# Kernel optimization log

Hardware: AMD Instinct MI355X
Metric: run time of the kernel (lower is better)

Reference implementation:

```python
import jax, jax.numpy as jnp
import numpy as np

B, L, H = 4, 1024, 8192
NH, HD = 64, 128
PD = HD // 2  # 64, rope-style positional dim
QL = HD * 4 * 3  # 1536, Q latent dim
KVL = HD * 4     # 512, KV latent dim


def setup_inputs() -> dict:
    key = jax.random.key(0)
    ks = jax.random.split(key, 18)
    w = lambda k, i, o: (jax.random.normal(k, (i, o), jnp.float32) * (1.0 / np.sqrt(i))).astype(jnp.float32)
    b = lambda k, o: jnp.zeros((o,), jnp.float32)
    return {
        'x': jax.random.normal(ks[0], (B, L, H), jnp.float32),
        'W_dq': w(ks[1], H, QL),   'b_dq': b(ks[2], QL),
        'W_dkv': w(ks[3], H, KVL), 'b_dkv': b(ks[4], KVL),
        'W_uq': w(ks[5], QL, H),   'b_uq': b(ks[6], H),
        'W_uk': w(ks[7], KVL, H),  'b_uk': b(ks[8], H),
        'W_uv': w(ks[9], KVL, H),  'b_uv': b(ks[10], H),
        'W_pq': w(ks[11], QL, NH * PD), 'b_pq': b(ks[12], NH * PD),
        'W_pk': w(ks[13], H, PD),  'b_pk': b(ks[14], PD),
        'W_o': w(ks[15], H, H),    'b_o': b(ks[16], H),
    }


def reference(x, W_dq, b_dq, W_dkv, b_dkv, W_uq, b_uq, W_uk, b_uk,
              W_uv, b_uv, W_pq, b_pq, W_pk, b_pk, W_o, b_o):
    Bb, Ll, Hh = x.shape
    # low-rank latents
    Q_lat = x @ W_dq + b_dq          # (B, L, 1536)
    KV_lat = x @ W_dkv + b_dkv       # (B, L, 512)
    # up-projections
    Q_c = (Q_lat @ W_uq + b_uq).reshape(Bb, Ll, NH, HD)
    Q_r = (Q_lat @ W_pq + b_pq).reshape(Bb, Ll, NH, PD)
    Q = jnp.concatenate([Q_c, Q_r], axis=-1)            # (B, L, NH, 192)
    K_c = (KV_lat @ W_uk + b_uk).reshape(Bb, Ll, NH, HD)
    K_r = x @ W_pk + b_pk                                # (B, L, 64), shared across heads
    K_r = jnp.broadcast_to(K_r[:, :, None, :], (Bb, Ll, NH, PD))
    K = jnp.concatenate([K_c, K_r], axis=-1)             # (B, L, NH, 192)
    V = (KV_lat @ W_uv + b_uv).reshape(Bb, Ll, NH, HD)   # (B, L, NH, 128)
    # attention with mismatched Q/K (192) vs V (128) head dims; scale by sqrt(128)
    scores = jnp.einsum('bqhd,bkhd->bhqk', Q, K) / np.float32(np.sqrt(HD))
    causal = jnp.tril(jnp.ones((Ll, Ll), bool))
    scores = jnp.where(causal, scores, jnp.float32(-jnp.inf))
    attn = jax.nn.softmax(scores, axis=-1)               # dropout = identity (eval)
    out = jnp.einsum('bhqk,bkhd->bqhd', attn, V).reshape(Bb, Ll, Hh)
    return out @ W_o + b_o
```

## Files before the change

### kernel.cpp

```cpp
#include <hip/hip_runtime.h>
#include <cstdint>

typedef unsigned short u16;
typedef __attribute__((ext_vector_type(8))) short bf16x8;
typedef __attribute__((ext_vector_type(4))) float f32x4;
typedef __attribute__((ext_vector_type(4))) unsigned short u16x4;

__device__ __forceinline__ u16 f2b(float f) {
  union { float f; uint32_t u; } v; v.f = f;
  uint32_t r = v.u + 0x7FFFu + ((v.u >> 16) & 1u);
  return (u16)(r >> 16);
}

__device__ __forceinline__ void gload_lds16(const void* g, void* l) {
  __builtin_amdgcn_global_load_lds((const __attribute__((address_space(1))) void*)g,
                                   (__attribute__((address_space(3))) void*)l, 16, 0, 0);
}

__device__ __forceinline__ void barrier_raw() {
  __builtin_amdgcn_sched_barrier(0);
  asm volatile("" ::: "memory");
  __builtin_amdgcn_s_barrier();
  asm volatile("" ::: "memory");
  __builtin_amdgcn_sched_barrier(0);
}
__device__ __forceinline__ void wait_vm8() {
  asm volatile("s_waitcnt vmcnt(8)" ::: "memory");
  __builtin_amdgcn_sched_barrier(0);
}

__global__ __launch_bounds__(256) void cvt_bf16(const float* __restrict__ in,
                                                u16* __restrict__ out, long n) {
  long i = ((long)blockIdx.x * 256 + threadIdx.x) * 4;
  if (i >= n) return;
  f32x4 v = *(const f32x4*)(in + i);
  u16x4 o;
#pragma unroll
  for (int k = 0; k < 4; k++) o[k] = f2b(v[k]);
  *(u16x4*)(out + i) = o;
}

__global__ __launch_bounds__(256) void transpose_cvt(const float* __restrict__ W,
                                                     u16* __restrict__ WT, int K, int N) {
  __shared__ float tile[32][33];
  const int tn0 = blockIdx.x * 32;
  const int tk0 = blockIdx.y * 32;
  const int c = threadIdx.x & 31;
  const int r0 = threadIdx.x >> 5;
#pragma unroll
  for (int rr = 0; rr < 32; rr += 8)
    tile[r0 + rr][c] = W[(long)(tk0 + r0 + rr) * N + tn0 + c];
  __syncthreads();
#pragma unroll
  for (int rr = 0; rr < 32; rr += 8)
    WT[(long)(tn0 + r0 + rr) * K + tk0 + c] = f2b(tile[c][r0 + rr]);
}

__global__ __launch_bounds__(256) void biascat(const float* __restrict__ a,
                                               const float* __restrict__ b,
                                               const float* __restrict__ c,
                                               float* __restrict__ o) {
  int i = blockIdx.x * 256 + threadIdx.x;
  if (i < 1536) o[i] = a[i];
  else if (i < 2048) o[i] = b[i - 1536];
  else if (i < 2112) o[i] = c[i - 2048];
}

__global__ __launch_bounds__(256) void repl_kr(const u16* __restrict__ Kr,
                                               u16* __restrict__ Kbuf, int stride) {
  long idx = (long)blockIdx.x * 256 + threadIdx.x;
  int d4 = idx & 15;
  long t = idx >> 4;
  int hh = t & 63;
  long tok = t >> 6;
  if (tok >= 4096) return;
  u16x4 v = *(const u16x4*)(Kr + tok * (long)stride + d4 * 4);
  long b = tok >> 10, l = tok & 1023;
  *(u16x4*)(Kbuf + ((b * 64 + hh) * 1024 + l) * 192 + 128 + d4 * 4) = v;
}

template<int MODE>
__global__ __launch_bounds__(512, 2) void gemm256(
    const u16* __restrict__ A, long lda, const u16* __restrict__ BT,
    const float* __restrict__ bias, void* __restrict__ outp,
    int N, int K, int p0, int p1) {
  __shared__ u16 sA[2][2][8192];
  __shared__ u16 sB[2][2][8192];
  const int tid = threadIdx.x;
  const int lane = tid & 63;
  const int w = tid >> 6;
  const int wr = w >> 2, wc = w & 3;
  const int hi = lane >> 4, lo = lane & 15;

  const int Nt = gridDim.x, Mt = gridDim.y;
  const int bid = blockIdx.y * Nt + blockIdx.x;
  const int xcd = bid & 7;
  const int idx = bid >> 3;
  int mt, nt;
  if ((Nt & 1) == 0) {
    const int Rm = Mt >> 2, Rn = Nt >> 1;
    const int xr = xcd & 3, xcn = xcd >> 2;
    const int Wb = Rn < 8 ? Rn : 8;
    const int cb = idx / (Rm * Wb);
    const int rem = idx - cb * (Rm * Wb);
    mt = xr * Rm + (rem % Rm);
    nt = xcn * Rn + cb * Wb + rem / Rm;
  } else {
    const int Rm = Mt >> 3;
    const int Wb = Nt < 8 ? Nt : 8;
    const int cb = idx / (Rm * Wb);
    const int rem = idx - cb * (Rm * Wb);
    mt = xcd * Rm + (rem % Rm);
    nt = cb * Wb + rem / Rm;
  }
  const long m0 = (long)mt * 256;
  const long n0 = (long)nt * 256;

  const int nkt = K >> 6;

  const int srow = tid >> 2;
  const int scol = ((tid & 3) ^ ((tid >> 3) & 3)) * 8;
  const long arow0 = m0 + srow, arow1 = arow0 + 128;
  long brow0 = n0 + srow, brow1 = brow0 + 128;
  if (brow0 > N - 1) brow0 = N - 1;
  if (brow1 > N - 1) brow1 = N - 1;
  const u16* aS0 = A + arow0 * lda + scol;
  const u16* aS1 = A + arow1 * lda + scol;
  const u16* bS0 = BT + brow0 * (long)K + scol;
  const u16* bS1 = BT + brow1 * (long)K + scol;

  const int aRd = (wr * 128 + lo) * 32 + (hi ^ ((lo >> 1) & 3)) * 8;
  const int bRd = (wc * 64 + lo) * 32 + (hi ^ ((lo >> 1) & 3)) * 8;

  f32x4 acc[8][4] = {};

#define STAGE(s0, s1, koff, dst) do { \
    gload_lds16((s0) + (koff), (dst) + tid * 8); \
    gload_lds16((s1) + (koff), (dst) + 4096 + tid * 8); \
  } while (0)
#define LDA_F(bufr, kh, m) (*(const bf16x8*)(&sA[bufr][kh][aRd + (m) * 512]))
#define LDB_F(bufr, kh, n) (*(const bf16x8*)(&sB[bufr][kh][bRd + (n) * 512]))
#define MFMA_GRP(mi, av) \
    acc[mi][0] = __builtin_amdgcn_mfma_f32_16x16x32_bf16(av, b0, acc[mi][0], 0, 0, 0); \
    acc[mi][1] = __builtin_amdgcn_mfma_f32_16x16x32_bf16(av, b1, acc[mi][1], 0, 0, 0); \
    acc[mi][2] = __builtin_amdgcn_mfma_f32_16x16x32_bf16(av, b2, acc[mi][2], 0, 0, 0); \
    acc[mi][3] = __builtin_amdgcn_mfma_f32_16x16x32_bf16(av, b3, acc[mi][3], 0, 0, 0);

  STAGE(aS0, aS1, 0, &sA[0][0][0]);
  STAGE(bS0, bS1, 0, &sB[0][0][0]);
  STAGE(aS0, aS1, 32, &sA[0][1][0]);
  STAGE(bS0, bS1, 32, &sB[0][1][0]);
  {
    const long t1o = (nkt > 1) ? 64 : 0;
    STAGE(aS0, aS1, t1o, &sA[1][0][0]);
    STAGE(bS0, bS1, t1o, &sB[1][0][0]);
  }
  asm volatile("s_waitcnt vmcnt(4)" ::: "memory");
  __builtin_amdgcn_sched_barrier(0);
  barrier_raw();

  for (int t = 0; t < nkt; ++t) {
    const int cur = t & 1, nxt = cur ^ 1;
    const int t1c = (t + 1 < nkt) ? t + 1 : nkt - 1;
    const int t2c = (t + 2 < nkt) ? t + 2 : nkt - 1;
    const long o1 = (long)t1c * 64;
    const long o2 = (long)t2c * 64;
    bf16x8 b0, b1, b2, b3, a0, a1, a2, a3;
    b0 = LDB_F(cur, 0, 0); b1 = LDB_F(cur, 0, 1); b2 = LDB_F(cur, 0, 2); b3 = LDB_F(cur, 0, 3);
    a0 = LDA_F(cur, 0, 0); a1 = LDA_F(cur, 0, 1); a2 = LDA_F(cur, 0, 2); a3 = LDA_F(cur, 0, 3);
    STAGE(aS0, aS1, o1 + 32, &sA[nxt][1][0]);
    barrier_raw();
    __builtin_amdgcn_s_setprio(1);
    MFMA_GRP(0, a0) MFMA_GRP(1, a1) MFMA_GRP(2, a2) MFMA_GRP(3, a3)
    __builtin_amdgcn_s_setprio(0);
    barrier_raw();
    a0 = LDA_F(cur, 0, 4); a1 = LDA_F(cur, 0, 5); a2 = LDA_F(cur, 0, 6); a3 = LDA_F(cur, 0, 7);
    STAGE(bS0, bS1, o1 + 32, &sB[nxt][1][0]);
    barrier_raw();
    __builtin_amdgcn_s_setprio(1);
    MFMA_GRP(4, a0) MFMA_GRP(5, a1) MFMA_GRP(6, a2) MFMA_GRP(7, a3)
    __builtin_amdgcn_s_setprio(0);
    wait_vm8();
    barrier_raw();
    b0 = LDB_F(cur, 1, 0); b1 = LDB_F(cur, 1, 1); b2 = LDB_F(cur, 1, 2); b3 = LDB_F(cur, 1, 3);
    a0 = LDA_F(cur, 1, 0); a1 = LDA_F(cur, 1, 1); a2 = LDA_F(cur, 1, 2); a3 = LDA_F(cur, 1, 3);
    STAGE(aS0, aS1, o2, &sA[cur][0][0]);
    barrier_raw();
    __builtin_amdgcn_s_setprio(1);
    MFMA_GRP(0, a0) MFMA_GRP(1, a1) MFMA_GRP(2, a2) MFMA_GRP(3, a3)
    __builtin_amdgcn_s_setprio(0);
    barrier_raw();
    a0 = LDA_F(cur, 1, 4); a1 = LDA_F(cur, 1, 5); a2 = LDA_F(cur, 1, 6); a3 = LDA_F(cur, 1, 7);
    STAGE(bS0, bS1, o2, &sB[cur][0][0]);
    barrier_raw();
    __builtin_amdgcn_s_setprio(1);
    MFMA_GRP(4, a0) MFMA_GRP(5, a1) MFMA_GRP(6, a2) MFMA_GRP(7, a3)
    __builtin_amdgcn_s_setprio(0);
    wait_vm8();
    barrier_raw();
  }
  asm volatile("s_waitcnt vmcnt(0)" ::: "memory");

#undef STAGE
#undef LDA_F
#undef LDB_F
#undef MFMA_GRP

#pragma unroll
  for (int m = 0; m < 8; m++) {
#pragma unroll
    for (int n = 0; n < 4; n++) {
      const long mb = m0 + wr * 128 + m * 16 + hi * 4;
      const long nn = n0 + wc * 64 + n * 16 + lo;
      if (nn >= N) continue;
      const float bv = bias[nn];
      if (MODE == 2) {
        u16x4 pk;
#pragma unroll
        for (int r = 0; r < 4; r++) pk[r] = f2b(acc[m][n][r] + bv);
        const long bq = mb >> 10, l = mb & 1023;
        const long h = nn >> 7, d = nn & 127;
        *(u16x4*)((u16*)outp + ((bq * 64 + h) * 128 + d) * 1024 + l) = pk;
      } else if (MODE == 1) {
#pragma unroll
        for (int r = 0; r < 4; r++) {
          const long mm = mb + r;
          const long bq = mm >> 10, l = mm & 1023;
          const long h = nn >> p0, d = nn & ((1 << p0) - 1);
          ((u16*)outp)[((bq * 64 + h) * 1024 + l) * 192 + p1 + d] = f2b(acc[m][n][r] + bv);
        }
      } else if (MODE == 3) {
#pragma unroll
        for (int r = 0; r < 4; r++)
          ((float*)outp)[(mb + r) * (long)N + nn] = acc[m][n][r] + bv;
      } else {
#pragma unroll
        for (int r = 0; r < 4; r++)
          ((u16*)outp)[(mb + r) * (long)N + nn] = f2b(acc[m][n][r] + bv);
      }
    }
  }
}

__global__ __launch_bounds__(512, 2) void attn256(const u16* __restrict__ Qb,
                                                  const u16* __restrict__ Kb,
                                                  const u16* __restrict__ Vt,
                                                  u16* __restrict__ O) {
  __shared__ u16 sK[2][12288];
  __shared__ u16 sV[2][8192];
  __shared__ u16 P[8][32][72];
  const int bh = blockIdx.x;
  const int qtb = 3 - blockIdx.y;
  const int b = bh >> 6, h = bh & 63;
  const int tid = threadIdx.x, w = tid >> 6, lane = tid & 63;
  const int hi = lane >> 4, lo = lane & 15, lo7 = lane & 7;
  const int q0w = qtb * 256 + w * 32;
  const u16* Qh = Qb + (size_t)bh * 1024 * 192;
  const u16* Kh = Kb + (size_t)bh * 1024 * 192;
  const u16* Vh = Vt + (size_t)bh * 128 * 1024;
  const float scale = 0.08838834764831845f;
  const float NEGINF = -3.0e38f;

  int kOff0, kOff1, kOff2, vOff0, vOff1;
  {
    int g0 = tid, g1 = tid + 512, g2 = tid + 1024;
    int r0 = g0 / 24, r1 = g1 / 24, r2 = g2 / 24;
    kOff0 = r0 * 192 + ((g0 - r0 * 24) ^ (r0 & 7)) * 8;
    kOff1 = r1 * 192 + ((g1 - r1 * 24) ^ (r1 & 7)) * 8;
    kOff2 = r2 * 192 + ((g2 - r2 * 24) ^ (r2 & 7)) * 8;
    int s0 = tid, s1 = tid + 512;
    vOff0 = (s0 >> 3) * 1024 + ((s0 & 7) ^ ((s0 >> 3) & 7)) * 8;
    vOff1 = (s1 >> 3) * 1024 + ((s1 & 7) ^ ((s1 >> 3) & 7)) * 8;
  }
#define STAGE_KV(tt, bb) do { \
    const u16* kb_ = Kh + (size_t)(tt) * (64 * 192); \
    const u16* vb_ = Vh + (size_t)(tt) * 64; \
    gload_lds16(kb_ + kOff0, &sK[bb][0] + tid * 8); \
    gload_lds16(kb_ + kOff1, &sK[bb][4096] + tid * 8); \
    gload_lds16(kb_ + kOff2, &sK[bb][8192] + tid * 8); \
    gload_lds16(vb_ + vOff0, &sV[bb][0] + tid * 8); \
    gload_lds16(vb_ + vOff1, &sV[bb][4096] + tid * 8); \
  } while (0)

  bf16x8 qf[2][6];
#pragma unroll
  for (int qi = 0; qi < 2; qi++) {
    const u16* qp = Qh + (size_t)(q0w + qi * 16 + lo) * 192 + hi * 8;
#pragma unroll
    for (int f = 0; f < 6; f++) qf[qi][f] = *(const bf16x8*)(qp + f * 32);
  }

  f32x4 oacc[2][8] = {};
  float m_run[2][4], l_run[2][4];
#pragma unroll
  for (int qi = 0; qi < 2; qi++)
#pragma unroll
    for (int r = 0; r < 4; r++) { m_run[qi][r] = NEGINF; l_run[qi][r] = 0.f; }

  const int nkt = (qtb + 1) * 4;
  STAGE_KV(0, 0);
  __syncthreads();

  for (int t = 0; t < nkt; t++) {
    const int cur = t & 1;
    const int tn = (t + 1 < nkt) ? t + 1 : nkt - 1;
    STAGE_KV(tn, cur ^ 1);
    const int k0 = t * 64;
    if (k0 < q0w + 32) {
      f32x4 s[2][4] = {};
      __builtin_amdgcn_s_setprio(1);
#pragma unroll
      for (int j = 0; j < 4; j++) {
#pragma unroll
        for (int f = 0; f < 6; f++) {
          bf16x8 kf = *(const bf16x8*)(&sK[cur][((j * 16 + lo) * 24 + ((f * 4 + hi) ^ lo7)) * 8]);
          s[0][j] = __builtin_amdgcn_mfma_f32_16x16x32_bf16(qf[0][f], kf, s[0][j], 0, 0, 0);
          s[1][j] = __builtin_amdgcn_mfma_f32_16x16x32_bf16(qf[1][f], kf, s[1][j], 0, 0, 0);
        }
      }
      __builtin_amdgcn_s_setprio(0);
      const bool diag = (k0 + 63 > q0w);
#pragma unroll
      for (int qi = 0; qi < 2; qi++) {
#pragma unroll
        for (int r = 0; r < 4; r++) {
          const int q = q0w + qi * 16 + hi * 4 + r;
          float sv[4];
          float mx = NEGINF;
#pragma unroll
          for (int j = 0; j < 4; j++) {
            float v = s[qi][j][r] * scale;
            if (diag && (k0 + j * 16 + lo > q)) v = NEGINF;
            sv[j] = v;
            mx = fmaxf(mx, v);
          }
#pragma unroll
          for (int o = 1; o < 16; o <<= 1) mx = fmaxf(mx, __shfl_xor(mx, o, 64));
          const float mnew = fmaxf(m_run[qi][r], mx);
          float sum = 0.f;
#pragma unroll
          for (int j = 0; j < 4; j++) {
            float pv = __expf(sv[j] - mnew);
            sum += pv;
            P[w][qi * 16 + hi * 4 + r][j * 16 + lo] = f2b(pv);
          }
#pragma unroll
          for (int o = 1; o < 16; o <<= 1) sum += __shfl_xor(sum, o, 64);
          const float alpha = __expf(m_run[qi][r] - mnew);
          l_run[qi][r] = l_run[qi][r] * alpha + sum;
          m_run[qi][r] = mnew;
#pragma unroll
          for (int j = 0; j < 8; j++) oacc[qi][j][r] *= alpha;
        }
      }
      __builtin_amdgcn_s_setprio(1);
#pragma unroll
      for (int kk = 0; kk < 2; kk++) {
        bf16x8 pf0 = *(const bf16x8*)(&P[w][lo][kk * 32 + hi * 8]);
        bf16x8 pf1 = *(const bf16x8*)(&P[w][16 + lo][kk * 32 + hi * 8]);
#pragma unroll
        for (int j = 0; j < 8; j++) {
          bf16x8 vf = *(const bf16x8*)(&sV[cur][((j * 16 + lo) * 8 + ((kk * 4 + hi) ^ lo7)) * 8]);
          oacc[0][j] = __builtin_amdgcn_mfma_f32_16x16x32_bf16(pf0, vf, oacc[0][j], 0, 0, 0);
          oacc[1][j] = __builtin_amdgcn_mfma_f32_16x16x32_bf16(pf1, vf, oacc[1][j], 0, 0, 0);
        }
      }
      __builtin_amdgcn_s_setprio(0);
    }
    __syncthreads();
  }
#undef STAGE_KV

#pragma unroll
  for (int qi = 0; qi < 2; qi++) {
#pragma unroll
    for (int r = 0; r < 4; r++) {
      const float inv = 1.f / l_run[qi][r];
      const int q = q0w + qi * 16 + hi * 4 + r;
      u16* op = O + ((size_t)(b * 1024 + q) * 64 + h) * 128;
#pragma unroll
      for (int j = 0; j < 8; j++)
        op[j * 16 + lo] = f2b(oacc[qi][j][r] * inv);
    }
  }
}

extern "C" void kernel_launch(void* const* d_in, const int* in_sizes, int n_in,
                              void* d_out, int out_size, void* d_ws, size_t ws_size,
                              hipStream_t stream) {
  const float* x     = (const float*)d_in[0];
  const float* W_dq  = (const float*)d_in[1];
  const float* b_dq  = (const float*)d_in[2];
  const float* W_dkv = (const float*)d_in[3];
  const float* b_dkv = (const float*)d_in[4];
  const float* W_uq  = (const float*)d_in[5];
  const float* b_uq  = (const float*)d_in[6];
  const float* W_uk  = (const float*)d_in[7];
  const float* b_uk  = (const float*)d_in[8];
  const float* W_uv  = (const float*)d_in[9];
  const float* b_uv  = (const float*)d_in[10];
  const float* W_pq  = (const float*)d_in[11];
  const float* b_pq  = (const float*)d_in[12];
  const float* W_pk  = (const float*)d_in[13];
  const float* b_pk  = (const float*)d_in[14];
  const float* W_o   = (const float*)d_in[15];
  const float* b_o   = (const float*)d_in[16];

  char* ws = (char*)d_ws;
  size_t off = 0;
  auto alloc = [&](size_t bytes) {
    char* p = ws + off;
    off += (bytes + 255) & ~(size_t)255;
    return p;
  };
  u16* xbf   = (u16*)alloc(33554432ULL * 2);
  u16* WT    = (u16*)alloc(67108864ULL * 2);
  u16* lat   = (u16*)alloc(4096ULL * 2112 * 2);
  float* bct = (float*)alloc(2112ULL * 4);
  u16* Qbuf  = (u16*)alloc(100663296ULL);
  u16* Kbuf  = (u16*)alloc(100663296ULL);
  u16* Vt    = (u16*)alloc(67108864ULL);
  u16* Obuf  = xbf;
  if (off > ws_size) return;

  dim3 blk(256), blk5(512);
  cvt_bf16<<<dim3(32768), blk, 0, stream>>>(x, xbf, 33554432L);
  transpose_cvt<<<dim3(48, 256), blk, 0, stream>>>(W_dq, WT, 8192, 1536);
  transpose_cvt<<<dim3(16, 256), blk, 0, stream>>>(W_dkv, WT + 1536L * 8192, 8192, 512);
  transpose_cvt<<<dim3(2, 256), blk, 0, stream>>>(W_pk, WT + 2048L * 8192, 8192, 64);
  biascat<<<dim3(9), blk, 0, stream>>>(b_dq, b_dkv, b_pk, bct);
  gemm256<0><<<dim3(9, 16), blk5, 0, stream>>>(xbf, 8192, WT, bct, lat, 2112, 8192, 0, 0);
  repl_kr<<<dim3(16384), blk, 0, stream>>>(lat + 2048, Kbuf, 2112);
  transpose_cvt<<<dim3(256, 48), blk, 0, stream>>>(W_uq, WT, 1536, 8192);
  gemm256<1><<<dim3(32, 16), blk5, 0, stream>>>(lat, 2112, WT, b_uq, Qbuf, 8192, 1536, 7, 0);
  transpose_cvt<<<dim3(128, 48), blk, 0, stream>>>(W_pq, WT, 1536, 4096);
  gemm256<1><<<dim3(16, 16), blk5, 0, stream>>>(lat, 2112, WT, b_pq, Qbuf, 4096, 1536, 6, 128);
  transpose_cvt<<<dim3(256, 16), blk, 0, stream>>>(W_uk, WT, 512, 8192);
  gemm256<1><<<dim3(32, 16), blk5, 0, stream>>>(lat + 1536, 2112, WT, b_uk, Kbuf, 8192, 512, 7, 0);
  transpose_cvt<<<dim3(256, 16), blk, 0, stream>>>(W_uv, WT, 512, 8192);
  gemm256<2><<<dim3(32, 16), blk5, 0, stream>>>(lat + 1536, 2112, WT, b_uv, Vt, 8192, 512, 0, 0);
  attn256<<<dim3(256, 4), blk5, 0, stream>>>(Qbuf, Kbuf, Vt, Obuf);
  transpose_cvt<<<dim3(256, 256), blk, 0, stream>>>(W_o, WT, 8192, 8192);
  gemm256<3><<<dim3(32, 16), blk5, 0, stream>>>(Obuf, 8192, WT, b_o, d_out, 8192, 8192, 0, 0);
}
```

Baseline: 1.446 ms.

## Fuse Q up-projections and K/V up-projections into wide GEMMs, trim GEMM barriers

After: 1.381 ms (median of 2 runs). 4.4% less time.

```diff
diff --git a/kernel.cpp b/kernel.cpp
--- a/kernel.cpp
+++ b/kernel.cpp
@@ -56,14 +56,21 @@
     WT[(long)(tn0 + r0 + rr) * K + tk0 + c] = f2b(tile[c][r0 + rr]);
 }
 
-__global__ __launch_bounds__(256) void biascat(const float* __restrict__ a,
-                                               const float* __restrict__ b,
-                                               const float* __restrict__ c,
-                                               float* __restrict__ o) {
+__global__ __launch_bounds__(256) void biascat3(const float* __restrict__ a,
+                                                const float* __restrict__ b,
+                                                const float* __restrict__ c,
+                                                float* __restrict__ o) {
   int i = blockIdx.x * 256 + threadIdx.x;
   if (i < 1536) o[i] = a[i];
   else if (i < 2048) o[i] = b[i - 1536];
   else if (i < 2112) o[i] = c[i - 2048];
+}
+__global__ __launch_bounds__(256) void biascat2(const float* __restrict__ a,
+                                                const float* __restrict__ b,
+                                                int na, int n, float* __restrict__ o) {
+  int i = blockIdx.x * 256 + threadIdx.x;
+  if (i >= n) return;
+  o[i] = (i < na) ? a[i] : b[i - na];
 }
 
 __global__ __launch_bounds__(256) void repl_kr(const u16* __restrict__ Kr,
@@ -82,8 +89,8 @@
 template<int MODE>
 __global__ __launch_bounds__(512, 2) void gemm256(
     const u16* __restrict__ A, long lda, const u16* __restrict__ BT,
-    const float* __restrict__ bias, void* __restrict__ outp,
-    int N, int K, int p0, int p1) {
+    const float* __restrict__ bias, void* __restrict__ outp, void* __restrict__ outp2,
+    int N, int K) {
   __shared__ u16 sA[2][2][8192];
   __shared__ u16 sB[2][2][8192];
   const int tid = threadIdx.x;
@@ -155,8 +162,7 @@
     STAGE(aS0, aS1, t1o, &sA[1][0][0]);
     STAGE(bS0, bS1, t1o, &sB[1][0][0]);
   }
-  asm volatile("s_waitcnt vmcnt(4)" ::: "memory");
-  __builtin_amdgcn_sched_barrier(0);
+  wait_vm8();
   barrier_raw();
 
   for (int t = 0; t < nkt; ++t) {
@@ -165,36 +171,32 @@
     const int t2c = (t + 2 < nkt) ? t + 2 : nkt - 1;
     const long o1 = (long)t1c * 64;
     const long o2 = (long)t2c * 64;
-    bf16x8 b0, b1, b2, b3, a0, a1, a2, a3;
+    bf16x8 b0, b1, b2, b3, a0, a1, a2, a3, a4, a5, a6, a7;
     b0 = LDB_F(cur, 0, 0); b1 = LDB_F(cur, 0, 1); b2 = LDB_F(cur, 0, 2); b3 = LDB_F(cur, 0, 3);
     a0 = LDA_F(cur, 0, 0); a1 = LDA_F(cur, 0, 1); a2 = LDA_F(cur, 0, 2); a3 = LDA_F(cur, 0, 3);
+    a4 = LDA_F(cur, 0, 4); a5 = LDA_F(cur, 0, 5); a6 = LDA_F(cur, 0, 6); a7 = LDA_F(cur, 0, 7);
     STAGE(aS0, aS1, o1 + 32, &sA[nxt][1][0]);
     barrier_raw();
     __builtin_amdgcn_s_setprio(1);
     MFMA_GRP(0, a0) MFMA_GRP(1, a1) MFMA_GRP(2, a2) MFMA_GRP(3, a3)
     __builtin_amdgcn_s_setprio(0);
-    barrier_raw();
-    a0 = LDA_F(cur, 0, 4); a1 = LDA_F(cur, 0, 5); a2 = LDA_F(cur, 0, 6); a3 = LDA_F(cur, 0, 7);
     STAGE(bS0, bS1, o1 + 32, &sB[nxt][1][0]);
-    barrier_raw();
     __builtin_amdgcn_s_setprio(1);
-    MFMA_GRP(4, a0) MFMA_GRP(5, a1) MFMA_GRP(6, a2) MFMA_GRP(7, a3)
+    MFMA_GRP(4, a4) MFMA_GRP(5, a5) MFMA_GRP(6, a6) MFMA_GRP(7, a7)
     __builtin_amdgcn_s_setprio(0);
     wait_vm8();
     barrier_raw();
     b0 = LDB_F(cur, 1, 0); b1 = LDB_F(cur, 1, 1); b2 = LDB_F(cur, 1, 2); b3 = LDB_F(cur, 1, 3);
     a0 = LDA_F(cur, 1, 0); a1 = LDA_F(cur, 1, 1); a2 = LDA_F(cur, 1, 2); a3 = LDA_F(cur, 1, 3);
+    a4 = LDA_F(cur, 1, 4); a5 = LDA_F(cur, 1, 5); a6 = LDA_F(cur, 1, 6); a7 = LDA_F(cur, 1, 7);
     STAGE(aS0, aS1, o2, &sA[cur][0][0]);
     barrier_raw();
     __builtin_amdgcn_s_setprio(1);
     MFMA_GRP(0, a0) MFMA_GRP(1, a1) MFMA_GRP(2, a2) MFMA_GRP(3, a3)
     __builtin_amdgcn_s_setprio(0);
-    barrier_raw();
-    a0 = LDA_F(cur, 1, 4); a1 = LDA_F(cur, 1, 5); a2 = LDA_F(cur, 1, 6); a3 = LDA_F(cur, 1, 7);
     STAGE(bS0, bS1, o2, &sB[cur][0][0]);
-    barrier_raw();
     __builtin_amdgcn_s_setprio(1);
-    MFMA_GRP(4, a0) MFMA_GRP(5, a1) MFMA_GRP(6, a2) MFMA_GRP(7, a3)
+    MFMA_GRP(4, a4) MFMA_GRP(5, a5) MFMA_GRP(6, a6) MFMA_GRP(7, a7)
     __builtin_amdgcn_s_setprio(0);
     wait_vm8();
     barrier_raw();
@@ -214,29 +216,51 @@
       const long nn = n0 + wc * 64 + n * 16 + lo;
       if (nn >= N) continue;
       const float bv = bias[nn];
-      if (MODE == 2) {
-        u16x4 pk;
-#pragma unroll
-        for (int r = 0; r < 4; r++) pk[r] = f2b(acc[m][n][r] + bv);
-        const long bq = mb >> 10, l = mb & 1023;
-        const long h = nn >> 7, d = nn & 127;
-        *(u16x4*)((u16*)outp + ((bq * 64 + h) * 128 + d) * 1024 + l) = pk;
-      } else if (MODE == 1) {
-#pragma unroll
-        for (int r = 0; r < 4; r++) {
-          const long mm = mb + r;
-          const long bq = mm >> 10, l = mm & 1023;
-          const long h = nn >> p0, d = nn & ((1 << p0) - 1);
-          ((u16*)outp)[((bq * 64 + h) * 1024 + l) * 192 + p1 + d] = f2b(acc[m][n][r] + bv);
-        }
+      if (MODE == 0) {
+#pragma unroll
+        for (int r = 0; r < 4; r++)
+          ((u16*)outp)[(mb + r) * (long)N + nn] = f2b(acc[m][n][r] + bv);
       } else if (MODE == 3) {
 #pragma unroll
         for (int r = 0; r < 4; r++)
           ((float*)outp)[(mb + r) * (long)N + nn] = acc[m][n][r] + bv;
+      } else if (MODE == 4) {
+        if (nn < 8192) {
+          const long h = nn >> 7, d = nn & 127;
+#pragma unroll
+          for (int r = 0; r < 4; r++) {
+            const long mm = mb + r;
+            const long bq = mm >> 10, l = mm & 1023;
+            ((u16*)outp)[((bq * 64 + h) * 1024 + l) * 192 + d] = f2b(acc[m][n][r] + bv);
+          }
+        } else {
+          const long q = nn - 8192;
+          const long h = q >> 6, d = q & 63;
+#pragma unroll
+          for (int r = 0; r < 4; r++) {
+            const long mm = mb + r;
+            const long bq = mm >> 10, l = mm & 1023;
+            ((u16*)outp)[((bq * 64 + h) * 1024 + l) * 192 + 128 + d] = f2b(acc[m][n][r] + bv);
+          }
+        }
       } else {
-#pragma unroll
-        for (int r = 0; r < 4; r++)
-          ((u16*)outp)[(mb + r) * (long)N + nn] = f2b(acc[m][n][r] + bv);
+        if (nn < 8192) {
+          const long h = nn >> 7, d = nn & 127;
+#pragma unroll
+          for (int r = 0; r < 4; r++) {
+            const long mm = mb + r;
+            const long bq = mm >> 10, l = mm & 1023;
+            ((u16*)outp)[((bq * 64 + h) * 1024 + l) * 192 + d] = f2b(acc[m][n][r] + bv);
+          }
+        } else {
+          const long v = nn - 8192;
+          const long h = v >> 7, d = v & 127;
+          u16x4 pk;
+#pragma unroll
+          for (int r = 0; r < 4; r++) pk[r] = f2b(acc[m][n][r] + bv);
+          const long bq = mb >> 10, l = mb & 1023;
+          *(u16x4*)((u16*)outp2 + ((bq * 64 + h) * 128 + d) * 1024 + l) = pk;
+        }
       }
     }
   }
@@ -417,6 +441,8 @@
   u16* WT    = (u16*)alloc(67108864ULL * 2);
   u16* lat   = (u16*)alloc(4096ULL * 2112 * 2);
   float* bct = (float*)alloc(2112ULL * 4);
+  float* bq  = (float*)alloc(12288ULL * 4);
+  float* bkv = (float*)alloc(16384ULL * 4);
   u16* Qbuf  = (u16*)alloc(100663296ULL);
   u16* Kbuf  = (u16*)alloc(100663296ULL);
   u16* Vt    = (u16*)alloc(67108864ULL);
@@ -428,18 +454,18 @@
   transpose_cvt<<<dim3(48, 256), blk, 0, stream>>>(W_dq, WT, 8192, 1536);
   transpose_cvt<<<dim3(16, 256), blk, 0, stream>>>(W_dkv, WT + 1536L * 8192, 8192, 512);
   transpose_cvt<<<dim3(2, 256), blk, 0, stream>>>(W_pk, WT + 2048L * 8192, 8192, 64);
-  biascat<<<dim3(9), blk, 0, stream>>>(b_dq, b_dkv, b_pk, bct);
-  gemm256<0><<<dim3(9, 16), blk5, 0, stream>>>(xbf, 8192, WT, bct, lat, 2112, 8192, 0, 0);
+  biascat3<<<dim3(9), blk, 0, stream>>>(b_dq, b_dkv, b_pk, bct);
+  gemm256<0><<<dim3(9, 16), blk5, 0, stream>>>(xbf, 8192, WT, bct, lat, nullptr, 2112, 8192);
   repl_kr<<<dim3(16384), blk, 0, stream>>>(lat + 2048, Kbuf, 2112);
   transpose_cvt<<<dim3(256, 48), blk, 0, stream>>>(W_uq, WT, 1536, 8192);
-  gemm256<1><<<dim3(32, 16), blk5, 0, stream>>>(lat, 2112, WT, b_uq, Qbuf, 8192, 1536, 7, 0);
-  transpose_cvt<<<dim3(128, 48), blk, 0, stream>>>(W_pq, WT, 1536, 4096);
-  gemm256<1><<<dim3(16, 16), blk5, 0, stream>>>(lat, 2112, WT, b_pq, Qbuf, 4096, 1536, 6, 128);
+  transpose_cvt<<<dim3(128, 48), blk, 0, stream>>>(W_pq, WT + 8192L * 1536, 1536, 4096);
+  biascat2<<<dim3(48), blk, 0, stream>>>(b_uq, b_pq, 8192, 12288, bq);
+  gemm256<4><<<dim3(48, 16), blk5, 0, stream>>>(lat, 2112, WT, bq, Qbuf, nullptr, 12288, 1536);
   transpose_cvt<<<dim3(256, 16), blk, 0, stream>>>(W_uk, WT, 512, 8192);
-  gemm256<1><<<dim3(32, 16), blk5, 0, stream>>>(lat + 1536, 2112, WT, b_uk, Kbuf, 8192, 512, 7, 0);
-  transpose_cvt<<<dim3(256, 16), blk, 0, stream>>>(W_uv, WT, 512, 8192);
-  gemm256<2><<<dim3(32, 16), blk5, 0, stream>>>(lat + 1536, 2112, WT, b_uv, Vt, 8192, 512, 0, 0);
+  transpose_cvt<<<dim3(256, 16), blk, 0, stream>>>(W_uv, WT + 8192L * 512, 512, 8192);
+  biascat2<<<dim3(64), blk, 0, stream>>>(b_uk, b_uv, 8192, 16384, bkv);
+  gemm256<5><<<dim3(64, 16), blk5, 0, stream>>>(lat + 1536, 2112, WT, bkv, Kbuf, Vt, 16384, 512);
   attn256<<<dim3(256, 4), blk5, 0, stream>>>(Qbuf, Kbuf, Vt, Obuf);
   transpose_cvt<<<dim3(256, 256), blk, 0, stream>>>(W_o, WT, 8192, 8192);
-  gemm256<3><<<dim3(32, 16), blk5, 0, stream>>>(Obuf, 8192, WT, b_o, d_out, 8192, 8192, 0, 0);
-}
+  gemm256<3><<<dim3(32, 16), blk5, 0, stream>>>(Obuf, 8192, WT, b_o, d_out, nullptr, 8192, 8192);
+}
```
